# Kernel optimization log

Measured on AMD Instinct MI355X. Metric: run time of the kernel, lower is better.

Reference implementation:

```python
import jax, jax.numpy as jnp
import numpy as np

N = 50000      # nodes
E = 600000     # edges (before self-loops)
F_IN = 128     # num_node_features
HID = 64       # hidden_channels
HEADS = 4      # num_heads
ACT = 32       # action_dim
SENT = 768     # sentence embedding dim (fc1 input)


def setup_inputs() -> dict:
    key = jax.random.key(0)
    ks = jax.random.split(key, 32)
    rn = lambda k, s, sc=0.05: jax.random.normal(k, s, jnp.float32) * sc
    return {
        "x": jax.random.normal(ks[0], (N, F_IN), jnp.float32),
        "edge_index": jax.random.randint(ks[1], (2, E), 0, N, dtype=jnp.int32),
        "sentence_emb": jax.random.normal(ks[2], (1, SENT), jnp.float32),
        "active_node_idx": 123,
        "step": 3,
        # conv1: GATConv(F_IN -> HID, heads=HEADS, concat=True)
        "W1": rn(ks[3], (F_IN, HEADS * HID)),
        "att_src1": rn(ks[4], (HEADS, HID)),
        "att_dst1": rn(ks[5], (HEADS, HID)),
        "b1": jnp.zeros((HEADS * HID,), jnp.float32),
        # conv2: GATConv(HEADS*HID -> HID, heads=1, concat=False)
        "W2": rn(ks[6], (HEADS * HID, HID)),
        "att_src2": rn(ks[7], (1, HID)),
        "att_dst2": rn(ks[8], (1, HID)),
        "b2": jnp.zeros((HID,), jnp.float32),
        "fc0_w": rn(ks[9], (1, HID)), "fc0_b": jnp.zeros((HID,), jnp.float32),
        "fc1_w": rn(ks[10], (SENT, HID)), "fc1_b": jnp.zeros((HID,), jnp.float32),
        "fc2_w": rn(ks[11], (HID, HID)), "fc2_b": jnp.zeros((HID,), jnp.float32),
        "fc3_w": rn(ks[12], (2 * HID, HID)), "fc3_b": jnp.zeros((HID,), jnp.float32),
        "val_w": rn(ks[13], (HID, 1)), "val_b": jnp.zeros((1,), jnp.float32),
        "adv_w": rn(ks[14], (HID, ACT)), "adv_b": jnp.zeros((ACT,), jnp.float32),
        "ln_h_g": jnp.ones((HID,), jnp.float32), "ln_h_b": jnp.zeros((HID,), jnp.float32),
        "ln_f_g": jnp.ones((2 * HID,), jnp.float32), "ln_f_b": jnp.zeros((2 * HID,), jnp.float32),
        "ln_a_g": jnp.ones((HEADS * HID,), jnp.float32), "ln_a_b": jnp.zeros((HEADS * HID,), jnp.float32),
    }


def layernorm(x, g, b, eps=1e-5):
    mu = jnp.mean(x, axis=-1, keepdims=True)
    var = jnp.mean((x - mu) ** 2, axis=-1, keepdims=True)
    return (x - mu) / jnp.sqrt(var + eps) * g + b


def gat_layer(h_in, src, dst, W, a_src, a_dst, bias, concat):
    """PyG GATConv (eval mode): gather -> edge score -> segment softmax -> scatter-add."""
    n = h_in.shape[0]
    heads, ch = a_src.shape
    h = (h_in @ W).reshape(n, heads, ch)                      # [N,H,C]
    es = jnp.einsum('nhc,hc->nh', h, a_src)                   # alpha_src per node
    ed = jnp.einsum('nhc,hc->nh', h, a_dst)                   # alpha_dst per node
    e = jax.nn.leaky_relu(es[src] + ed[dst], 0.2)             # [Etot,H]
    m = jax.ops.segment_max(e, dst, num_segments=n)           # stable softmax per dst
    ex = jnp.exp(e - m[dst])
    denom = jax.ops.segment_sum(ex, dst, num_segments=n) + 1e-16
    alpha = ex / denom[dst]                                   # [Etot,H]
    out = jax.ops.segment_sum(h[src] * alpha[:, :, None], dst, num_segments=n)
    out = out.reshape(n, heads * ch) if concat else out.mean(axis=1)
    return out + bias, alpha


def reference(x, edge_index, sentence_emb, active_node_idx, step,
              W1, att_src1, att_dst1, b1, W2, att_src2, att_dst2, b2,
              fc0_w, fc0_b, fc1_w, fc1_b, fc2_w, fc2_b, fc3_w, fc3_b,
              val_w, val_b, adv_w, adv_b,
              ln_h_g, ln_h_b, ln_f_g, ln_f_b, ln_a_g, ln_a_b):
    n = x.shape[0]
    loops = jnp.arange(n, dtype=edge_index.dtype)             # PyG add_self_loops=True
    src = jnp.concatenate([edge_index[0], loops])
    dst = jnp.concatenate([edge_index[1], loops])

    # step embedding: fc0((step+1)*0.01) -> relu -> LN
    steps = jnp.full((1, 1), (step + 1) * 0.01, jnp.float32)
    steps = layernorm(jax.nn.relu(steps @ fc0_w + fc0_b), ln_h_g, ln_h_b)

    # sentence embedding path (F.normalize result is discarded in the original)
    sent = layernorm(jax.nn.relu(sentence_emb @ fc1_w + fc1_b), ln_h_g, ln_h_b)
    sent = sent + steps
    sent = layernorm(jax.nn.relu(sent @ fc2_w + fc2_b), ln_h_g, ln_h_b)

    # two GAT layers
    h1, _ = gat_layer(x, src, dst, W1, att_src1, att_dst1, b1, concat=True)
    h1 = layernorm(jax.nn.elu(h1), ln_a_g, ln_a_b)
    h2, alpha = gat_layer(h1, src, dst, W2, att_src2, att_dst2, b2, concat=False)
    h2 = layernorm(h2, ln_h_g, ln_h_b)

    # dueling head on active node
    anf = jnp.concatenate([h2[active_node_idx][None, :], sent], axis=1)   # [1, 2*HID]
    anf = layernorm(anf, ln_f_g, ln_f_b)
    anf = layernorm(jax.nn.relu(anf @ fc3_w + fc3_b), ln_h_g, ln_h_b)
    val = anf @ val_w + val_b
    adv = anf @ adv_w + adv_b
    logits = jnp.tanh(val + adv - adv.mean())
    return logits, h2, alpha
```

## Files before the change

kernel.cpp:

```cpp
#include <hip/hip_runtime.h>
#include <cstdint>
#include <cstddef>

#define DEV __device__ __forceinline__

static constexpr int NN  = 50000;
static constexpr int EE  = 600000;
static constexpr int ET  = 650000;
static constexpr int CAP = 96;

typedef __attribute__((ext_vector_type(8))) short bf16x8;
typedef __attribute__((ext_vector_type(4))) float f32x4;
typedef __attribute__((ext_vector_type(4))) int   i32x4;

DEV float wsum(float v){
  #pragma unroll
  for (int o = 32; o > 0; o >>= 1) v += __shfl_xor(v, o, 64);
  return v;
}
DEV float wmaxr(float v){
  #pragma unroll
  for (int o = 32; o > 0; o >>= 1) v = fmaxf(v, __shfl_xor(v, o, 64));
  return v;
}
DEV float lrelu(float x){ return x > 0.f ? x : 0.2f * x; }
DEV float eluf(float x){ return x > 0.f ? x : expm1f(x); }
DEV float ln64(float v, const float* g, const float* b, int lane){
  float mu  = wsum(v) * (1.f/64.f);
  float d   = v - mu;
  float var = wsum(d*d) * (1.f/64.f);
  return d * rsqrtf(var + 1e-5f) * g[lane] + b[lane];
}
DEV unsigned int bf16u(float f){
  unsigned int u = __float_as_uint(f);
  return (u + 0x7fffu + ((u >> 16) & 1u)) >> 16;
}
DEV float bfl(unsigned int lo16){ return __uint_as_float(lo16 << 16); }

__global__ void bucket_fill(const int* __restrict__ ei,
                            int* __restrict__ cnt,
                            int2* __restrict__ bucket){
  int e = blockIdx.x * blockDim.x + threadIdx.x;
  if (e >= ET) return;
  int src, dst;
  if (e < EE){ src = ei[e]; dst = ei[EE + e]; } else { src = dst = e - EE; }
  int pos = atomicAdd(&cnt[dst], 1);
  if (pos < CAP) bucket[(size_t)dst * CAP + pos] = make_int2(src, e);
}

__global__ __launch_bounds__(256) void pack_both(const float* __restrict__ W1,
                                                 const float* __restrict__ W2,
                                                 short* __restrict__ Wp1,
                                                 short* __restrict__ Wp2){
  int tid = blockIdx.x * 256 + threadIdx.x;
  if (tid < 4096){
    int lane = tid & 63, ks = (tid >> 6) & 3, mb = tid >> 8;
    int col  = mb * 16 + (lane & 15);
    int krow = ks * 32 + (lane >> 4) * 8;
    #pragma unroll
    for (int j = 0; j < 8; j++)
      Wp1[(size_t)tid * 8 + j] = (short)bf16u(W1[(size_t)(krow + j) * 256 + col]);
  } else if (tid < 4096 + 2048){
    int t2 = tid - 4096;
    int lane = t2 & 63, ks = (t2 >> 6) & 7, mb = t2 >> 9;
    int col  = mb * 16 + (lane & 15);
    int krow = ks * 32 + (lane >> 4) * 8;
    #pragma unroll
    for (int j = 0; j < 8; j++)
      Wp2[(size_t)t2 * 8 + j] = (short)bf16u(W2[(size_t)(krow + j) * 64 + col]);
  }
}

template<int KSTEPS, int MBLKS, int NH, bool INF32>
__global__ __launch_bounds__(256) void mfma_gemm_att(const short* __restrict__ Wp,
                                                     const float* __restrict__ Xf,
                                                     const unsigned short* __restrict__ Xh,
                                                     unsigned short* __restrict__ Cb,
                                                     const float* __restrict__ asrc,
                                                     const float* __restrict__ adst,
                                                     float* __restrict__ es,
                                                     float* __restrict__ ed, int M){
  constexpr int K = KSTEPS * 32, N = MBLKS * 16;
  int lane  = threadIdx.x & 63;
  int wv    = threadIdx.x >> 6;
  int quad  = lane >> 4;
  int node  = blockIdx.x * 64 + wv * 16 + (lane & 15);
  bool nv   = node < M;
  int nodec = nv ? node : M - 1;

  f32x4 acc[MBLKS];
  #pragma unroll
  for (int m = 0; m < MBLKS; m++) acc[m] = (f32x4){0.f, 0.f, 0.f, 0.f};

  #pragma unroll
  for (int ks = 0; ks < KSTEPS; ks++){
    int k0 = ks * 32 + quad * 8;
    bf16x8 bfrag;
    if (INF32){
      float4 u = *(const float4*)(Xf + (size_t)nodec * K + k0);
      float4 v = *(const float4*)(Xf + (size_t)nodec * K + k0 + 4);
      i32x4 bi;
      bi.x = (int)(bf16u(u.x) | (bf16u(u.y) << 16));
      bi.y = (int)(bf16u(u.z) | (bf16u(u.w) << 16));
      bi.z = (int)(bf16u(v.x) | (bf16u(v.y) << 16));
      bi.w = (int)(bf16u(v.z) | (bf16u(v.w) << 16));
      bfrag = __builtin_bit_cast(bf16x8, bi);
    } else {
      bfrag = *(const bf16x8*)(Xh + (size_t)nodec * K + k0);
    }
    #pragma unroll
    for (int mb = 0; mb < MBLKS; mb++){
      bf16x8 afrag = *(const bf16x8*)(Wp + ((size_t)(mb * KSTEPS + ks) * 64 + lane) * 8);
      acc[mb] = __builtin_amdgcn_mfma_f32_16x16x32_bf16(afrag, bfrag, acc[mb], 0, 0, 0);
    }
  }

  if (nv){
    unsigned short* crow = Cb + (size_t)node * N;
    #pragma unroll
    for (int mb = 0; mb < MBLKS; mb++){
      uint2 p;
      p.x = bf16u(acc[mb][0]) | (bf16u(acc[mb][1]) << 16);
      p.y = bf16u(acc[mb][2]) | (bf16u(acc[mb][3]) << 16);
      *(uint2*)(crow + mb * 16 + quad * 4) = p;
    }
  }

  float ps[NH], pd[NH];
  #pragma unroll
  for (int h = 0; h < NH; h++){ ps[h] = 0.f; pd[h] = 0.f; }
  #pragma unroll
  for (int mb = 0; mb < MBLKS; mb++){
    int h = (NH == 1) ? 0 : (mb >> 2);
    #pragma unroll
    for (int r = 0; r < 4; r++){
      int c = mb * 16 + quad * 4 + r;
      ps[h] = fmaf(acc[mb][r], asrc[c], ps[h]);
      pd[h] = fmaf(acc[mb][r], adst[c], pd[h]);
    }
  }
  #pragma unroll
  for (int h = 0; h < NH; h++){
    ps[h] += __shfl_xor(ps[h], 16, 64); ps[h] += __shfl_xor(ps[h], 32, 64);
    pd[h] += __shfl_xor(pd[h], 16, 64); pd[h] += __shfl_xor(pd[h], 32, 64);
  }
  if (quad == 0 && nv){
    if (NH == 4){
      *(float4*)(es + (size_t)node * 4) = make_float4(ps[0], ps[1], ps[2], ps[3]);
      *(float4*)(ed + (size_t)node * 4) = make_float4(pd[0], pd[1], pd[2], pd[3]);
    } else {
      es[node] = ps[0];
      ed[node] = pd[0];
    }
  }
}

DEV void acc4u(uint2 g, float q, float& ax, float& ay, float& az, float& aw){
  ax = fmaf(__uint_as_float(g.x << 16),         q, ax);
  ay = fmaf(__uint_as_float(g.x & 0xffff0000u), q, ay);
  az = fmaf(__uint_as_float(g.y << 16),         q, az);
  aw = fmaf(__uint_as_float(g.y & 0xffff0000u), q, aw);
}

__global__ __launch_bounds__(256) void agg1_kernel(const int* __restrict__ cnt,
                                                   const int2* __restrict__ bucket,
                                                   const unsigned short* __restrict__ H1b,
                                                   const float* __restrict__ es,
                                                   const float* __restrict__ ed,
                                                   const float* __restrict__ b1,
                                                   const float* __restrict__ lng,
                                                   const float* __restrict__ lnb,
                                                   unsigned short* __restrict__ h1b, int n){
  __shared__ float wsh4[4][64][4];
  __shared__ int   ssh[4][64];
  int wv   = threadIdx.x >> 6;
  int wid  = (blockIdx.x * blockDim.x + threadIdx.x) >> 6;
  int lane = threadIdx.x & 63;
  if (wid >= n) return;
  int deg = min(cnt[wid], CAP);
  const int2* base = bucket + (size_t)wid * CAP;
  const float4 edv = *(const float4*)(ed + (size_t)wid * 4);

  float v0, v1, v2, v3;

  if (deg <= 64){
    bool vld = lane < deg;
    int srcl = vld ? base[lane].x : 0;
    float4 e4 = vld ? *(const float4*)(es + (size_t)srcl * 4)
                    : make_float4(-1e30f, -1e30f, -1e30f, -1e30f);
    float e0 = vld ? lrelu(e4.x + edv.x) : -1e30f;
    float e1 = vld ? lrelu(e4.y + edv.y) : -1e30f;
    float e2 = vld ? lrelu(e4.z + edv.z) : -1e30f;
    float e3 = vld ? lrelu(e4.w + edv.w) : -1e30f;
    float m0 = wmaxr(e0), m1 = wmaxr(e1), m2 = wmaxr(e2), m3 = wmaxr(e3);
    float w0 = vld ? __expf(e0 - m0) : 0.f;
    float w1 = vld ? __expf(e1 - m1) : 0.f;
    float w2 = vld ? __expf(e2 - m2) : 0.f;
    float w3 = vld ? __expf(e3 - m3) : 0.f;
    w0 /= (wsum(w0) + 1e-16f);
    w1 /= (wsum(w1) + 1e-16f);
    w2 /= (wsum(w2) + 1e-16f);
    w3 /= (wsum(w3) + 1e-16f);
    ssh[wv][lane] = srcl;
    *(float4*)&wsh4[wv][lane][0] = make_float4(w0, w1, w2, w3);
    __builtin_amdgcn_wave_barrier();

    int h = lane >> 4;
    int lane4 = lane * 4;
    float ax = 0.f, ay = 0.f, az = 0.f, aw = 0.f;
    int t = 0;
    for (; t + 4 <= deg; t += 4){
      int a0 = ssh[wv][t],     a1 = ssh[wv][t + 1];
      int a2 = ssh[wv][t + 2], a3 = ssh[wv][t + 3];
      float q0 = wsh4[wv][t][h],     q1 = wsh4[wv][t + 1][h];
      float q2 = wsh4[wv][t + 2][h], q3 = wsh4[wv][t + 3][h];
      uint2 g0 = *(const uint2*)(H1b + (size_t)a0 * 256 + lane4);
      uint2 g1 = *(const uint2*)(H1b + (size_t)a1 * 256 + lane4);
      uint2 g2 = *(const uint2*)(H1b + (size_t)a2 * 256 + lane4);
      uint2 g3 = *(const uint2*)(H1b + (size_t)a3 * 256 + lane4);
      acc4u(g0, q0, ax, ay, az, aw);
      acc4u(g1, q1, ax, ay, az, aw);
      acc4u(g2, q2, ax, ay, az, aw);
      acc4u(g3, q3, ax, ay, az, aw);
    }
    for (; t < deg; t++){
      int a0 = ssh[wv][t];
      float q0 = wsh4[wv][t][h];
      uint2 g0 = *(const uint2*)(H1b + (size_t)a0 * 256 + lane4);
      acc4u(g0, q0, ax, ay, az, aw);
    }
    float4 bb = *(const float4*)(b1 + lane4);
    v0 = eluf(ax + bb.x); v1 = eluf(ay + bb.y);
    v2 = eluf(az + bb.z); v3 = eluf(aw + bb.w);
    float mu = wsum(v0 + v1 + v2 + v3) * (1.f/256.f);
    float q  = (v0-mu)*(v0-mu) + (v1-mu)*(v1-mu) + (v2-mu)*(v2-mu) + (v3-mu)*(v3-mu);
    float rstd = rsqrtf(wsum(q) * (1.f/256.f) + 1e-5f);
    float4 g4v = *(const float4*)(lng + lane4);
    float4 bo  = *(const float4*)(lnb + lane4);
    uint2 p;
    p.x = bf16u((v0-mu)*rstd*g4v.x + bo.x) | (bf16u((v1-mu)*rstd*g4v.y + bo.y) << 16);
    p.y = bf16u((v2-mu)*rstd*g4v.z + bo.z) | (bf16u((v3-mu)*rstd*g4v.w + bo.w) << 16);
    *(uint2*)(h1b + (size_t)wid * 256 + lane4) = p;
    return;
  }

  float m0 = -1e30f, m1 = -1e30f, m2 = -1e30f, m3 = -1e30f;
  for (int j = lane; j < deg; j += 64){
    int src = base[j].x;
    float4 e4 = *(const float4*)(es + (size_t)src * 4);
    m0 = fmaxf(m0, lrelu(e4.x + edv.x));
    m1 = fmaxf(m1, lrelu(e4.y + edv.y));
    m2 = fmaxf(m2, lrelu(e4.z + edv.z));
    m3 = fmaxf(m3, lrelu(e4.w + edv.w));
  }
  m0 = wmaxr(m0); m1 = wmaxr(m1); m2 = wmaxr(m2); m3 = wmaxr(m3);
  float acc0 = 0.f, acc1 = 0.f, acc2 = 0.f, acc3 = 0.f;
  float den0 = 0.f, den1 = 0.f, den2 = 0.f, den3 = 0.f;
  for (int j = 0; j < deg; j++){
    int src = base[j].x;
    float4 e4 = *(const float4*)(es + (size_t)src * 4);
    float x0 = __expf(lrelu(e4.x + edv.x) - m0);
    float x1 = __expf(lrelu(e4.y + edv.y) - m1);
    float x2 = __expf(lrelu(e4.z + edv.z) - m2);
    float x3 = __expf(lrelu(e4.w + edv.w) - m3);
    den0 += x0; den1 += x1; den2 += x2; den3 += x3;
    const unsigned short* hp = H1b + (size_t)src * 256;
    acc0 = fmaf(bfl(hp[lane]),       x0, acc0);
    acc1 = fmaf(bfl(hp[64 + lane]),  x1, acc1);
    acc2 = fmaf(bfl(hp[128 + lane]), x2, acc2);
    acc3 = fmaf(bfl(hp[192 + lane]), x3, acc3);
  }
  v0 = eluf(acc0 / (den0 + 1e-16f) + b1[lane]);
  v1 = eluf(acc1 / (den1 + 1e-16f) + b1[64 + lane]);
  v2 = eluf(acc2 / (den2 + 1e-16f) + b1[128 + lane]);
  v3 = eluf(acc3 / (den3 + 1e-16f) + b1[192 + lane]);
  float mu = wsum(v0 + v1 + v2 + v3) * (1.f/256.f);
  float q  = (v0-mu)*(v0-mu) + (v1-mu)*(v1-mu) + (v2-mu)*(v2-mu) + (v3-mu)*(v3-mu);
  float rstd = rsqrtf(wsum(q) * (1.f/256.f) + 1e-5f);
  unsigned short* o = h1b + (size_t)wid * 256;
  o[lane]       = (unsigned short)bf16u((v0-mu)*rstd*lng[lane]       + lnb[lane]);
  o[64 + lane]  = (unsigned short)bf16u((v1-mu)*rstd*lng[64 + lane]  + lnb[64 + lane]);
  o[128 + lane] = (unsigned short)bf16u((v2-mu)*rstd*lng[128 + lane] + lnb[128 + lane]);
  o[192 + lane] = (unsigned short)bf16u((v3-mu)*rstd*lng[192 + lane] + lnb[192 + lane]);
}

DEV float agg2_slow(const int2* base, int deg, float edv,
                    const unsigned short* H2b, const float* es,
                    float* alpha_out, int lane){
  float m = -1e30f;
  for (int j = lane; j < deg; j += 64)
    m = fmaxf(m, lrelu(es[base[j].x] + edv));
  m = wmaxr(m);
  float den = 0.f;
  for (int j = lane; j < deg; j += 64)
    den += __expf(lrelu(es[base[j].x] + edv) - m);
  den = wsum(den) + 1e-16f;
  float acc = 0.f;
  for (int j = 0; j < deg; j++){
    int2 be = base[j];
    float a = __expf(lrelu(es[be.x] + edv) - m) / den;
    if (lane == 0) alpha_out[be.y] = a;
    acc = fmaf(bfl(H2b[(size_t)be.x * 64 + lane]), a, acc);
  }
  return acc;
}

__global__ __launch_bounds__(256) void agg2_head(const int* __restrict__ cnt,
                                                 const int2* __restrict__ bucket,
                                                 const unsigned short* __restrict__ H2b,
                                                 const float* __restrict__ es,
                                                 const float* __restrict__ ed,
                                                 const float* __restrict__ b2,
                                                 const float* __restrict__ lng,
                                                 const float* __restrict__ lnb,
                                                 const float* __restrict__ semb,
                                                 const int* __restrict__ active,
                                                 const int* __restrict__ stepp,
                                                 const float* __restrict__ fc0w, const float* __restrict__ fc0b,
                                                 const float* __restrict__ fc1w, const float* __restrict__ fc1b,
                                                 const float* __restrict__ fc2w, const float* __restrict__ fc2b,
                                                 const float* __restrict__ fc3w, const float* __restrict__ fc3b,
                                                 const float* __restrict__ valw, const float* __restrict__ valb,
                                                 const float* __restrict__ advw, const float* __restrict__ advb,
                                                 const float* __restrict__ lnhg, const float* __restrict__ lnhb,
                                                 const float* __restrict__ lnfg, const float* __restrict__ lnfb,
                                                 float* __restrict__ h2out,
                                                 float* __restrict__ alpha_out,
                                                 float* __restrict__ logits, int n){
  __shared__ float shh[192];
  int wpair = (blockIdx.x * blockDim.x + threadIdx.x) >> 6;
  int lane  = threadIdx.x & 63;
  int n0 = wpair * 2, n1 = wpair * 2 + 1;
  if (n0 >= n) return;
  bool has1 = n1 < n;

  int deg0 = min(cnt[n0], CAP);
  int deg1 = has1 ? min(cnt[n1], CAP) : 0;
  const int2* base0 = bucket + (size_t)n0 * CAP;
  const int2* base1 = bucket + (size_t)n1 * CAP;
  float edv0 = ed[n0];
  float edv1 = has1 ? ed[n1] : 0.f;
  float acc0 = 0.f, acc1 = 0.f;

  if (deg0 <= 64 && deg1 <= 64){
    bool v0 = lane < deg0;
    int2 be0 = v0 ? base0[lane] : make_int2(0, 0);
    int s0 = v0 ? be0.x : 0;
    float e0 = v0 ? lrelu(es[s0] + edv0) : -1e30f;
    float m0 = wmaxr(e0);
    float w0 = v0 ? __expf(e0 - m0) : 0.f;
    float wl0 = w0 / (wsum(w0) + 1e-16f);
    if (v0) alpha_out[be0.y] = wl0;
    if (!v0) wl0 = 0.f;
    bool v1 = lane < deg1;
    int2 be1 = v1 ? base1[lane] : make_int2(0, 0);
    int s1 = v1 ? be1.x : 0;
    float e1 = v1 ? lrelu(es[s1] + edv1) : -1e30f;
    float m1 = wmaxr(e1);
    float w1 = v1 ? __expf(e1 - m1) : 0.f;
    float wl1 = w1 / (wsum(w1) + 1e-16f);
    if (v1) alpha_out[be1.y] = wl1;
    if (!v1) wl1 = 0.f;

    int dmax = max(deg0, deg1);
    int t = 0;
    for (; t + 2 <= dmax; t += 2){
      int a00 = __shfl(s0, t, 64),   a01 = __shfl(s0, t + 1, 64);
      int a10 = __shfl(s1, t, 64),   a11 = __shfl(s1, t + 1, 64);
      float q00 = __shfl(wl0, t, 64), q01 = __shfl(wl0, t + 1, 64);
      float q10 = __shfl(wl1, t, 64), q11 = __shfl(wl1, t + 1, 64);
      float h00 = bfl(H2b[(size_t)a00 * 64 + lane]);
      float h01 = bfl(H2b[(size_t)a01 * 64 + lane]);
      float h10 = bfl(H2b[(size_t)a10 * 64 + lane]);
      float h11 = bfl(H2b[(size_t)a11 * 64 + lane]);
      acc0 = fmaf(h00, q00, acc0); acc0 = fmaf(h01, q01, acc0);
      acc1 = fmaf(h10, q10, acc1); acc1 = fmaf(h11, q11, acc1);
    }
    for (; t < dmax; t++){
      int a00 = __shfl(s0, t, 64);
      int a10 = __shfl(s1, t, 64);
      float q00 = __shfl(wl0, t, 64);
      float q10 = __shfl(wl1, t, 64);
      acc0 = fmaf(bfl(H2b[(size_t)a00 * 64 + lane]), q00, acc0);
      acc1 = fmaf(bfl(H2b[(size_t)a10 * 64 + lane]), q10, acc1);
    }
  } else {
    acc0 = agg2_slow(base0, deg0, edv0, H2b, es, alpha_out, lane);
    if (has1) acc1 = agg2_slow(base1, deg1, edv1, H2b, es, alpha_out, lane);
  }

  float va = acc0 + b2[lane];
  float mua = wsum(va) * (1.f/64.f);
  float da = va - mua;
  float rsa = rsqrtf(wsum(da*da) * (1.f/64.f) + 1e-5f);
  float h2v0 = da * rsa * lng[lane] + lnb[lane];
  h2out[(size_t)n0 * 64 + lane] = h2v0;
  float h2v1 = 0.f;
  if (has1){
    float vb = acc1 + b2[lane];
    float mub = wsum(vb) * (1.f/64.f);
    float db = vb - mub;
    float rsb = rsqrtf(wsum(db*db) * (1.f/64.f) + 1e-5f);
    h2v1 = db * rsb * lng[lane] + lnb[lane];
    h2out[(size_t)n1 * 64 + lane] = h2v1;
  }

  int actv = active[0];
  if (n0 == actv || n1 == actv){
    int t = lane;
    float h2v = (n0 == actv) ? h2v0 : h2v1;

    float sval = (float)(stepp[0] + 1) * 0.01f;
    float stepsv = ln64(fmaxf(fmaf(sval, fc0w[t], fc0b[t]), 0.f), lnhg, lnhb, t);

    float acc1h = fc1b[t];
    #pragma unroll 8
    for (int k = 0; k < 768; k++) acc1h = fmaf(semb[k], fc1w[k * 64 + t], acc1h);
    float sentv = ln64(fmaxf(acc1h, 0.f), lnhg, lnhb, t) + stepsv;
    shh[t] = sentv;
    __builtin_amdgcn_wave_barrier();
    float acc2h = fc2b[t];
    #pragma unroll 8
    for (int k = 0; k < 64; k++) acc2h = fmaf(shh[k], fc2w[k * 64 + t], acc2h);
    __builtin_amdgcn_wave_barrier();
    float sent2 = ln64(fmaxf(acc2h, 0.f), lnhg, lnhb, t);

    float c0 = h2v, c1 = sent2;
    float mu2 = wsum(c0 + c1) * (1.f/128.f);
    float q2  = (c0-mu2)*(c0-mu2) + (c1-mu2)*(c1-mu2);
    float rs2 = rsqrtf(wsum(q2) * (1.f/128.f) + 1e-5f);
    shh[t]      = (c0-mu2)*rs2*lnfg[t]      + lnfb[t];
    shh[64 + t] = (c1-mu2)*rs2*lnfg[64 + t] + lnfb[64 + t];
    __builtin_amdgcn_wave_barrier();

    float acc3h = fc3b[t];
    #pragma unroll 8
    for (int k = 0; k < 128; k++) acc3h = fmaf(shh[k], fc3w[k * 64 + t], acc3h);
    float a2v = ln64(fmaxf(acc3h, 0.f), lnhg, lnhb, t);
    shh[128 + t] = a2v;
    __builtin_amdgcn_wave_barrier();

    float val = wsum(a2v * valw[t]) + valb[0];
    float advv = 0.f;
    if (t < 32){
      advv = advb[t];
      #pragma unroll 8
      for (int k = 0; k < 64; k++) advv = fmaf(shh[128 + k], advw[k * 32 + t], advv);
    }
    float am = wsum(t < 32 ? advv : 0.f) * (1.f/32.f);
    if (t < 32) logits[t] = tanhf(val + advv - am);
  }
}

extern "C" void kernel_launch(void* const* d_in, const int* in_sizes, int n_in,
                              void* d_out, int out_size, void* d_ws, size_t ws_size,
                              hipStream_t stream) {
  const float* x     = (const float*)d_in[0];
  const int*   ei    = (const int*)  d_in[1];
  const float* semb  = (const float*)d_in[2];
  const int*   act   = (const int*)  d_in[3];
  const int*   step  = (const int*)  d_in[4];
  const float* W1    = (const float*)d_in[5];
  const float* as1   = (const float*)d_in[6];
  const float* ad1   = (const float*)d_in[7];
  const float* b1    = (const float*)d_in[8];
  const float* W2    = (const float*)d_in[9];
  const float* as2   = (const float*)d_in[10];
  const float* ad2   = (const float*)d_in[11];
  const float* b2    = (const float*)d_in[12];
  const float* fc0w  = (const float*)d_in[13];
  const float* fc0b  = (const float*)d_in[14];
  const float* fc1w  = (const float*)d_in[15];
  const float* fc1b  = (const float*)d_in[16];
  const float* fc2w  = (const float*)d_in[17];
  const float* fc2b  = (const float*)d_in[18];
  const float* fc3w  = (const float*)d_in[19];
  const float* fc3b  = (const float*)d_in[20];
  const float* valw  = (const float*)d_in[21];
  const float* valb  = (const float*)d_in[22];
  const float* advw  = (const float*)d_in[23];
  const float* advb  = (const float*)d_in[24];
  const float* lnhg  = (const float*)d_in[25];
  const float* lnhb  = (const float*)d_in[26];
  const float* lnfg  = (const float*)d_in[27];
  const float* lnfb  = (const float*)d_in[28];
  const float* lnag  = (const float*)d_in[29];
  const float* lnab  = (const float*)d_in[30];

  char* ws = (char*)d_ws;
  size_t o = 0;
  auto alloc = [&](size_t bytes) -> void* {
    o = (o + 255) & ~(size_t)255;
    void* p = ws + o;
    o += bytes;
    return p;
  };
  int*   cnt     = (int*)  alloc((size_t)NN * 4);
  int2*  bucket  = (int2*) alloc((size_t)NN * CAP * 8);
  short* Wp1     = (short*)alloc((size_t)4096 * 8 * 2);
  short* Wp2     = (short*)alloc((size_t)2048 * 8 * 2);
  unsigned short* H1b = (unsigned short*)alloc((size_t)NN * 256 * 2);
  unsigned short* h1b = (unsigned short*)alloc((size_t)NN * 256 * 2);
  float* es1     = (float*)alloc((size_t)NN * 16);
  float* ed1     = (float*)alloc((size_t)NN * 16);
  unsigned short* H2b = H1b;
  float* es2 = es1;
  float* ed2 = ed1;

  float* logits    = (float*)d_out;
  float* h2out     = (float*)d_out + 32;
  float* alpha_out = (float*)d_out + 32 + (size_t)NN * 64;

  hipMemsetAsync(cnt, 0, (size_t)NN * 4, stream);
  bucket_fill<<<(ET + 255) / 256, 256, 0, stream>>>(ei, cnt, bucket);
  pack_both<<<24, 256, 0, stream>>>(W1, W2, Wp1, Wp2);

  mfma_gemm_att<4, 16, 4, true><<<(NN + 63) / 64, 256, 0, stream>>>(
      Wp1, x, nullptr, H1b, as1, ad1, es1, ed1, NN);
  agg1_kernel<<<NN / 4, 256, 0, stream>>>(cnt, bucket, H1b, es1, ed1, b1, lnag, lnab, h1b, NN);

  mfma_gemm_att<8, 4, 1, false><<<(NN + 63) / 64, 256, 0, stream>>>(
      Wp2, nullptr, h1b, H2b, as2, ad2, es2, ed2, NN);
  agg2_head<<<(NN + 7) / 8, 256, 0, stream>>>(cnt, bucket, H2b, es2, ed2, b2,
                                              lnhg, lnhb,
                                              semb, act, step,
                                              fc0w, fc0b, fc1w, fc1b, fc2w, fc2b, fc3w, fc3b,
                                              valw, valb, advw, advb,
                                              lnhg, lnhb, lnfg, lnfb,
                                              h2out, alpha_out, logits, NN);
}
```

Measured before the change: 359.2 us.

## Shrink bucket to src-only and compute edge alphas in a separate coalesced pass

The CSR bucket now stores only source indices instead of (src, edge id) pairs, which halves bucket memory traffic in both aggregation kernels. The second aggregation no longer scatters per-edge attention weights. It stores a per-node max and denominator instead, and a new edge-parallel kernel recomputes alpha for each edge in original edge order with coalesced writes. The cost is an extra launch and recomputing the edge scores with gathers from es/ed/mden. Edges beyond CAP now receive alpha values, where before they were not written.

```diff
diff --git a/kernel.cpp b/kernel.cpp
--- a/kernel.cpp
+++ b/kernel.cpp
@@ -39,13 +39,13 @@
 
 __global__ void bucket_fill(const int* __restrict__ ei,
                             int* __restrict__ cnt,
-                            int2* __restrict__ bucket){
+                            int* __restrict__ bucket){
   int e = blockIdx.x * blockDim.x + threadIdx.x;
   if (e >= ET) return;
   int src, dst;
   if (e < EE){ src = ei[e]; dst = ei[EE + e]; } else { src = dst = e - EE; }
   int pos = atomicAdd(&cnt[dst], 1);
-  if (pos < CAP) bucket[(size_t)dst * CAP + pos] = make_int2(src, e);
+  if (pos < CAP) bucket[(size_t)dst * CAP + pos] = src;
 }
 
 __global__ __launch_bounds__(256) void pack_both(const float* __restrict__ W1,
@@ -163,7 +163,7 @@
 }
 
 __global__ __launch_bounds__(256) void agg1_kernel(const int* __restrict__ cnt,
-                                                   const int2* __restrict__ bucket,
+                                                   const int* __restrict__ bucket,
                                                    const unsigned short* __restrict__ H1b,
                                                    const float* __restrict__ es,
                                                    const float* __restrict__ ed,
@@ -178,14 +178,14 @@
   int lane = threadIdx.x & 63;
   if (wid >= n) return;
   int deg = min(cnt[wid], CAP);
-  const int2* base = bucket + (size_t)wid * CAP;
+  const int* base = bucket + (size_t)wid * CAP;
   const float4 edv = *(const float4*)(ed + (size_t)wid * 4);
 
   float v0, v1, v2, v3;
 
   if (deg <= 64){
     bool vld = lane < deg;
-    int srcl = vld ? base[lane].x : 0;
+    int srcl = vld ? base[lane] : 0;
     float4 e4 = vld ? *(const float4*)(es + (size_t)srcl * 4)
                     : make_float4(-1e30f, -1e30f, -1e30f, -1e30f);
     float e0 = vld ? lrelu(e4.x + edv.x) : -1e30f;
@@ -246,7 +246,7 @@
 
   float m0 = -1e30f, m1 = -1e30f, m2 = -1e30f, m3 = -1e30f;
   for (int j = lane; j < deg; j += 64){
-    int src = base[j].x;
+    int src = base[j];
     float4 e4 = *(const float4*)(es + (size_t)src * 4);
     m0 = fmaxf(m0, lrelu(e4.x + edv.x));
     m1 = fmaxf(m1, lrelu(e4.y + edv.y));
@@ -257,7 +257,7 @@
   float acc0 = 0.f, acc1 = 0.f, acc2 = 0.f, acc3 = 0.f;
   float den0 = 0.f, den1 = 0.f, den2 = 0.f, den3 = 0.f;
   for (int j = 0; j < deg; j++){
-    int src = base[j].x;
+    int src = base[j];
     float4 e4 = *(const float4*)(es + (size_t)src * 4);
     float x0 = __expf(lrelu(e4.x + edv.x) - m0);
     float x1 = __expf(lrelu(e4.y + edv.y) - m1);
@@ -284,29 +284,29 @@
   o[192 + lane] = (unsigned short)bf16u((v3-mu)*rstd*lng[192 + lane] + lnb[192 + lane]);
 }
 
-DEV float agg2_slow(const int2* base, int deg, float edv,
+DEV float agg2_slow(const int* base, int deg, float edv,
                     const unsigned short* H2b, const float* es,
-                    float* alpha_out, int lane){
+                    int lane, float& m_out, float& den_out){
   float m = -1e30f;
   for (int j = lane; j < deg; j += 64)
-    m = fmaxf(m, lrelu(es[base[j].x] + edv));
+    m = fmaxf(m, lrelu(es[base[j]] + edv));
   m = wmaxr(m);
   float den = 0.f;
   for (int j = lane; j < deg; j += 64)
-    den += __expf(lrelu(es[base[j].x] + edv) - m);
+    den += __expf(lrelu(es[base[j]] + edv) - m);
   den = wsum(den) + 1e-16f;
   float acc = 0.f;
   for (int j = 0; j < deg; j++){
-    int2 be = base[j];
-    float a = __expf(lrelu(es[be.x] + edv) - m) / den;
-    if (lane == 0) alpha_out[be.y] = a;
-    acc = fmaf(bfl(H2b[(size_t)be.x * 64 + lane]), a, acc);
-  }
+    int src = base[j];
+    float a = __expf(lrelu(es[src] + edv) - m) / den;
+    acc = fmaf(bfl(H2b[(size_t)src * 64 + lane]), a, acc);
+  }
+  m_out = m; den_out = den;
   return acc;
 }
 
 __global__ __launch_bounds__(256) void agg2_head(const int* __restrict__ cnt,
-                                                 const int2* __restrict__ bucket,
+                                                 const int* __restrict__ bucket,
                                                  const unsigned short* __restrict__ H2b,
                                                  const float* __restrict__ es,
                                                  const float* __restrict__ ed,
@@ -325,7 +325,7 @@
                                                  const float* __restrict__ lnhg, const float* __restrict__ lnhb,
                                                  const float* __restrict__ lnfg, const float* __restrict__ lnfb,
                                                  float* __restrict__ h2out,
-                                                 float* __restrict__ alpha_out,
+                                                 float2* __restrict__ mden,
                                                  float* __restrict__ logits, int n){
   __shared__ float shh[192];
   int wpair = (blockIdx.x * blockDim.x + threadIdx.x) >> 6;
@@ -336,31 +336,31 @@
 
   int deg0 = min(cnt[n0], CAP);
   int deg1 = has1 ? min(cnt[n1], CAP) : 0;
-  const int2* base0 = bucket + (size_t)n0 * CAP;
-  const int2* base1 = bucket + (size_t)n1 * CAP;
+  const int* base0 = bucket + (size_t)n0 * CAP;
+  const int* base1 = bucket + (size_t)n1 * CAP;
   float edv0 = ed[n0];
   float edv1 = has1 ? ed[n1] : 0.f;
   float acc0 = 0.f, acc1 = 0.f;
 
   if (deg0 <= 64 && deg1 <= 64){
     bool v0 = lane < deg0;
-    int2 be0 = v0 ? base0[lane] : make_int2(0, 0);
-    int s0 = v0 ? be0.x : 0;
+    int s0 = v0 ? base0[lane] : 0;
     float e0 = v0 ? lrelu(es[s0] + edv0) : -1e30f;
     float m0 = wmaxr(e0);
     float w0 = v0 ? __expf(e0 - m0) : 0.f;
-    float wl0 = w0 / (wsum(w0) + 1e-16f);
-    if (v0) alpha_out[be0.y] = wl0;
-    if (!v0) wl0 = 0.f;
+    float den0 = wsum(w0) + 1e-16f;
+    float wl0 = v0 ? w0 / den0 : 0.f;
     bool v1 = lane < deg1;
-    int2 be1 = v1 ? base1[lane] : make_int2(0, 0);
-    int s1 = v1 ? be1.x : 0;
+    int s1 = v1 ? base1[lane] : 0;
     float e1 = v1 ? lrelu(es[s1] + edv1) : -1e30f;
     float m1 = wmaxr(e1);
     float w1 = v1 ? __expf(e1 - m1) : 0.f;
-    float wl1 = w1 / (wsum(w1) + 1e-16f);
-    if (v1) alpha_out[be1.y] = wl1;
-    if (!v1) wl1 = 0.f;
+    float den1 = wsum(w1) + 1e-16f;
+    float wl1 = v1 ? w1 / den1 : 0.f;
+    if (lane == 0){
+      mden[n0] = make_float2(m0, den0);
+      if (has1) mden[n1] = make_float2(m1, den1);
+    }
 
     int dmax = max(deg0, deg1);
     int t = 0;
@@ -385,8 +385,13 @@
       acc1 = fmaf(bfl(H2b[(size_t)a10 * 64 + lane]), q10, acc1);
     }
   } else {
-    acc0 = agg2_slow(base0, deg0, edv0, H2b, es, alpha_out, lane);
-    if (has1) acc1 = agg2_slow(base1, deg1, edv1, H2b, es, alpha_out, lane);
+    float m0, den0, m1 = 0.f, den1 = 1.f;
+    acc0 = agg2_slow(base0, deg0, edv0, H2b, es, lane, m0, den0);
+    if (has1) acc1 = agg2_slow(base1, deg1, edv1, H2b, es, lane, m1, den1);
+    if (lane == 0){
+      mden[n0] = make_float2(m0, den0);
+      if (has1) mden[n1] = make_float2(m1, den1);
+    }
   }
 
   float va = acc0 + b2[lane];
@@ -450,6 +455,20 @@
     float am = wsum(t < 32 ? advv : 0.f) * (1.f/32.f);
     if (t < 32) logits[t] = tanhf(val + advv - am);
   }
+}
+
+__global__ __launch_bounds__(256) void edge_alpha(const int* __restrict__ ei,
+                                                  const float* __restrict__ es,
+                                                  const float* __restrict__ ed,
+                                                  const float2* __restrict__ mden,
+                                                  float* __restrict__ alpha_out){
+  int e = blockIdx.x * blockDim.x + threadIdx.x;
+  if (e >= ET) return;
+  int src, dst;
+  if (e < EE){ src = ei[e]; dst = ei[EE + e]; } else { src = dst = e - EE; }
+  float2 md = mden[dst];
+  float sc = lrelu(es[src] + ed[dst]);
+  alpha_out[e] = __expf(sc - md.x) / md.y;
 }
 
 extern "C" void kernel_launch(void* const* d_in, const int* in_sizes, int n_in,
@@ -496,13 +515,14 @@
     return p;
   };
   int*   cnt     = (int*)  alloc((size_t)NN * 4);
-  int2*  bucket  = (int2*) alloc((size_t)NN * CAP * 8);
+  int*   bucket  = (int*)  alloc((size_t)NN * CAP * 4);
   short* Wp1     = (short*)alloc((size_t)4096 * 8 * 2);
   short* Wp2     = (short*)alloc((size_t)2048 * 8 * 2);
   unsigned short* H1b = (unsigned short*)alloc((size_t)NN * 256 * 2);
   unsigned short* h1b = (unsigned short*)alloc((size_t)NN * 256 * 2);
   float* es1     = (float*)alloc((size_t)NN * 16);
   float* ed1     = (float*)alloc((size_t)NN * 16);
+  float2* mden   = (float2*)alloc((size_t)NN * 8);
   unsigned short* H2b = H1b;
   float* es2 = es1;
   float* ed2 = ed1;
@@ -527,5 +547,6 @@
                                               fc0w, fc0b, fc1w, fc1b, fc2w, fc2b, fc3w, fc3b,
                                               valw, valb, advw, advb,
                                               lnhg, lnhb, lnfg, lnfb,
-                                              h2out, alpha_out, logits, NN);
-}
+                                              h2out, mden, logits, NN);
+  edge_alpha<<<(ET + 255) / 256, 256, 0, stream>>>(ei, es2, ed2, mden, alpha_out);
+}
```

Result: faster. 336.9 us (-6.2%).
